# Kernel tuning notes

Measured on AMD Instinct MI355X. Metric: run time of the kernel, lower is better.

## Reference

```python
import jax, jax.numpy as jnp
import numpy as np

B, T, D, H = 4, 2048, 512, 8
DK = D // H

def setup_inputs() -> dict:
    key = jax.random.key(0)
    ks = jax.random.split(key, 5)
    s = 1.0 / np.sqrt(D)
    return {
        "x": jax.random.normal(ks[0], (B, T, D), dtype=jnp.float32),
        "Wq": jax.random.normal(ks[1], (D, D), dtype=jnp.float32) * s,
        "bq": jnp.zeros((D,), dtype=jnp.float32),
        "Wk": jax.random.normal(ks[2], (D, D), dtype=jnp.float32) * s,
        "bk": jnp.zeros((D,), dtype=jnp.float32),
        "Wv": jax.random.normal(ks[3], (D, D), dtype=jnp.float32) * s,
        "bv": jnp.zeros((D,), dtype=jnp.float32),
        "Wo": jax.random.normal(ks[4], (D, D), dtype=jnp.float32) * s,
        "bo": jnp.zeros((D,), dtype=jnp.float32),
    }

def reference(x, Wq, bq, Wk, bk, Wv, bv, Wo, bo):
    # Linear projections (torch Linear: x @ W.T + b); split into heads.
    q = (x @ Wq.T + bq).reshape(B, T, H, DK)  # [B,T,H,dk]
    k = (x @ Wk.T + bk).reshape(B, T, H, DK)
    v = (x @ Wv.T + bv).reshape(B, T, H, DK)
    scale = 1.0 / np.sqrt(DK)
    # scores: [B,H,T,T]
    scores = jnp.einsum("bqhd,bkhd->bhqk", q, k) * scale
    attn = jax.nn.softmax(scores, axis=-1)
    ctx = jnp.einsum("bhqk,bkhd->bqhd", attn, v).reshape(B, T, D)
    return ctx @ Wo.T + bo
```

## Files before the change

### kernel.cpp

```cpp
#include <hip/hip_runtime.h>
#include <stdint.h>

#define NB 4
#define NT 2048
#define ND 512
#define NH 8
#define NDK 64
#define NM (NB*NT)

typedef __attribute__((ext_vector_type(8))) short short8;
typedef __attribute__((ext_vector_type(4))) short bs4;
typedef __attribute__((ext_vector_type(4))) float f32x4;

__device__ __forceinline__ unsigned short f2b(float f) {
    union { float f; uint32_t u; } v; v.f = f;
    return (unsigned short)((v.u + 0x7FFFu + ((v.u >> 16) & 1u)) >> 16);
}

__device__ __forceinline__ void load_lds16(const void* g, void* l) {
    void* gn = const_cast<void*>(g);
    __builtin_amdgcn_global_load_lds((__attribute__((address_space(1))) void*)gn,
                                     (__attribute__((address_space(3))) void*)l,
                                     16, 0, 0);
}

__global__ void convert_all(const float* __restrict__ x,  const float* __restrict__ wq,
                            const float* __restrict__ wk, const float* __restrict__ wv,
                            const float* __restrict__ wo, unsigned short* __restrict__ dst) {
    size_t i = ((size_t)blockIdx.x * 256 + threadIdx.x) * 4;
    const float* src; size_t off;
    if (i < 4194304) { src = x; off = i; }
    else {
        size_t j = i - 4194304;
        src = (j < 262144) ? wq : (j < 524288) ? wk : (j < 786432) ? wv : wo;
        off = j & 262143;
    }
    f32x4 v = *(const f32x4*)(src + off);
    ushort4 r;
    r.x = f2b(v[0]); r.y = f2b(v[1]); r.z = f2b(v[2]); r.w = f2b(v[3]);
    *(ushort4*)(dst + i) = r;
}

__global__ __launch_bounds__(256, 3) void proj_gemm(
        const unsigned short* __restrict__ X,
        const unsigned short* __restrict__ Wbase,
        const float* __restrict__ bias0, const float* __restrict__ bias1,
        const float* __restrict__ bias2,
        unsigned short* __restrict__ Obase, unsigned short* __restrict__ VTb,
        float scale0) {
    const int z = blockIdx.z;
    const float* bias = (z == 0) ? bias0 : (z == 1 ? bias1 : bias2);
    const float scale = (z == 0) ? scale0 : 1.0f;

    int rowBase, colBase;
    const unsigned short *Ap, *Bp;
    if (z == 2) {
        rowBase = blockIdx.x * 128;  colBase = blockIdx.y * 128;
        Ap = Wbase + 2 * (ND * ND);  Bp = X;
    } else {
        rowBase = blockIdx.y * 128;  colBase = blockIdx.x * 128;
        Ap = X;                      Bp = Wbase + (size_t)z * (ND * ND);
    }

    __shared__ alignas(16) unsigned short ldsA[128 * 32];
    __shared__ alignas(16) unsigned short ldsW[128 * 32];

    const int tid = threadIdx.x;
    const int lane = tid & 63, wave = tid >> 6;
    const int quad = lane >> 4, l15 = lane & 15;
    const int wm = wave >> 1, wn = wave & 1;

    const int rS = wave * 16 + (lane >> 2);
    const int kS = (lane & 3) * 8;
    const unsigned short* gA = Ap + (size_t)(rowBase + rS) * ND + kS;
    const unsigned short* gW = Bp + (size_t)(colBase + rS) * ND + kS;
    unsigned short* lA = ldsA + wave * 512;
    unsigned short* lW = ldsW + wave * 512;

    f32x4 acc[4][4];
#pragma unroll
    for (int i = 0; i < 4; i++)
#pragma unroll
        for (int j = 0; j < 4; j++) acc[i][j] = (f32x4)0.0f;

    for (int kt = 0; kt < ND / 32; ++kt) {
        __syncthreads();
        load_lds16(gA,            lA);
        load_lds16(gA + 64 * ND,  lA + 2048);
        load_lds16(gW,            lW);
        load_lds16(gW + 64 * ND,  lW + 2048);
        gA += 32; gW += 32;
        __syncthreads();

        short8 af[4], bfm[4];
#pragma unroll
        for (int mt = 0; mt < 4; ++mt)
            af[mt] = *(const short8*)(ldsA + (wm * 64 + mt * 16 + l15) * 32 + quad * 8);
#pragma unroll
        for (int nt = 0; nt < 4; ++nt)
            bfm[nt] = *(const short8*)(ldsW + (wn * 64 + nt * 16 + l15) * 32 + quad * 8);
#pragma unroll
        for (int mt = 0; mt < 4; ++mt)
#pragma unroll
            for (int nt = 0; nt < 4; ++nt)
                acc[mt][nt] = __builtin_amdgcn_mfma_f32_16x16x32_bf16(
                    af[mt], bfm[nt], acc[mt][nt], 0, 0, 0);
    }

    if (z == 2) {
        const int bz = colBase >> 11;
        const int t0 = colBase & 2047;
        unsigned short* VTo = VTb + ((size_t)(bz * 512 + rowBase)) * NT + t0;
#pragma unroll
        for (int mt = 0; mt < 4; mt++)
#pragma unroll
            for (int reg = 0; reg < 4; reg++) {
                int m = wm * 64 + mt * 16 + quad * 4 + reg;
                float bm = bias[rowBase + m];
                unsigned short* dst = VTo + (size_t)m * NT + wn * 64 + l15;
#pragma unroll
                for (int nt = 0; nt < 4; nt++)
                    dst[nt * 16] = f2b(acc[mt][nt][reg] + bm);
            }
    } else {
        float biasr[4];
#pragma unroll
        for (int nt = 0; nt < 4; nt++)
            biasr[nt] = bias[colBase + wn * 64 + nt * 16 + l15];
        unsigned short* Oz = Obase + (size_t)z * ((size_t)NM * ND);
#pragma unroll
        for (int mt = 0; mt < 4; mt++) {
            int row = rowBase + wm * 64 + mt * 16 + quad * 4;
#pragma unroll
            for (int reg = 0; reg < 4; reg++) {
                unsigned short* dst = Oz + (size_t)(row + reg) * ND + colBase + wn * 64 + l15;
#pragma unroll
                for (int nt = 0; nt < 4; nt++)
                    dst[nt * 16] = f2b((acc[mt][nt][reg] + biasr[nt]) * scale);
            }
        }
    }
}

__global__ __launch_bounds__(256, 4) void out_gemm(
        const unsigned short* __restrict__ A, const unsigned short* __restrict__ W,
        const float* __restrict__ bias, float* __restrict__ OF) {
    __shared__ alignas(16) unsigned short ldsA[64 * 32];
    __shared__ alignas(16) unsigned short ldsW[128 * 32];

    const int tid = threadIdx.x;
    const int lane = tid & 63, wave = tid >> 6;
    const int quad = lane >> 4, l15 = lane & 15;
    const int rowBase = blockIdx.y * 64;
    const int colBase = blockIdx.x * 128;

    const int rW = wave * 16 + (lane >> 2);
    const int kS = (lane & 3) * 8;
    const unsigned short* gA = A + (size_t)(rowBase + rW) * ND + kS;
    const unsigned short* gW = W + (size_t)(colBase + rW) * ND + kS;
    unsigned short* lA = ldsA + wave * 512;
    unsigned short* lW = ldsW + wave * 512;

    f32x4 acc[8];
#pragma unroll
    for (int nt = 0; nt < 8; nt++) acc[nt] = (f32x4)0.0f;

    for (int kt = 0; kt < ND / 32; ++kt) {
        __syncthreads();
        load_lds16(gA,           lA);
        load_lds16(gW,           lW);
        load_lds16(gW + 64 * ND, lW + 2048);
        gA += 32; gW += 32;
        __syncthreads();

        short8 af = *(const short8*)(ldsA + (wave * 16 + l15) * 32 + quad * 8);
#pragma unroll
        for (int nt = 0; nt < 8; ++nt) {
            short8 bfm = *(const short8*)(ldsW + (nt * 16 + l15) * 32 + quad * 8);
            acc[nt] = __builtin_amdgcn_mfma_f32_16x16x32_bf16(af, bfm, acc[nt], 0, 0, 0);
        }
    }

    float biasr[8];
#pragma unroll
    for (int nt = 0; nt < 8; nt++)
        biasr[nt] = bias[colBase + nt * 16 + l15];

#pragma unroll
    for (int reg = 0; reg < 4; reg++) {
        int row = rowBase + wave * 16 + quad * 4 + reg;
        float* dst = OF + (size_t)row * ND + colBase + l15;
#pragma unroll
        for (int nt = 0; nt < 8; nt++)
            dst[nt * 16] = acc[nt][reg] + biasr[nt];
    }
}

__global__ __launch_bounds__(256, 4) void attn_kernel(
        const unsigned short* __restrict__ Qb, const unsigned short* __restrict__ Kb,
        const unsigned short* __restrict__ VTb, unsigned short* __restrict__ Cb) {
    const int qt = blockIdx.x, h = blockIdx.y, b = blockIdx.z;
    __shared__ alignas(16) unsigned short Ks[64 * 64];
    __shared__ alignas(16) unsigned short Vt[64 * 64];

    const int tid = threadIdx.x, lane = tid & 63, wave = tid >> 6;
    const int quad = lane >> 4, l15 = lane & 15;
    const size_t headOff = (size_t)h * NDK;
    const size_t rowB = (size_t)b * NT;
    const unsigned short* VT = VTb + (size_t)(b * NH + h) * ((size_t)NDK * NT);

    short8 aq[2];
#pragma unroll
    for (int ks = 0; ks < 2; ++ks)
        aq[ks] = *(const short8*)(Qb + (rowB + qt * 64 + wave * 16 + l15) * ND
                                  + headOff + ks * 32 + quad * 8);

    const int r0 = wave * 16 + (lane >> 3);
    const int g0 = (lane & 7) ^ (r0 & 7);
    const unsigned short* Kbh = Kb + rowB * ND + headOff;
    const size_t offK0 = (size_t)r0 * ND + g0 * 8;
    const size_t offK1 = (size_t)(r0 + 8) * ND + g0 * 8;
    const size_t offV0 = (size_t)r0 * NT + g0 * 8;
    const size_t offV1 = (size_t)(r0 + 8) * NT + g0 * 8;
    unsigned short* ldsK = Ks + wave * 1024;
    unsigned short* ldsV = Vt + wave * 1024;

    const int swz = (l15 & 7);

    f32x4 o[4];
#pragma unroll
    for (int nt = 0; nt < 4; nt++) o[nt] = (f32x4)0.0f;
    float lacc = 0.0f;

    for (int kv = 0; kv < NT / 64; ++kv) {
        const unsigned short* kb = Kbh + (size_t)kv * 64 * ND;
        const unsigned short* vb = VT + kv * 64;
        __syncthreads();
        load_lds16(kb + offK0, ldsK);
        load_lds16(kb + offK1, ldsK + 512);
        load_lds16(vb + offV0, ldsV);
        load_lds16(vb + offV1, ldsV + 512);
        __syncthreads();

        bs4 pk[4];
#pragma unroll
        for (int kt = 0; kt < 4; ++kt) {
            f32x4 st = (f32x4)0.0f;
#pragma unroll
            for (int ks = 0; ks < 2; ++ks) {
                short8 ak = *(const short8*)&Ks[(kt * 16 + l15) * 64
                                                + (((ks * 4 + quad) ^ swz) * 8)];
                st = __builtin_amdgcn_mfma_f32_16x16x32_bf16(ak, aq[ks], st, 0, 0, 0);
            }
            float p0 = exp2f(st[0]), p1 = exp2f(st[1]);
            float p2 = exp2f(st[2]), p3 = exp2f(st[3]);
            lacc += (p0 + p1) + (p2 + p3);
            uint32_t lo = __builtin_amdgcn_perm(__float_as_uint(p1), __float_as_uint(p0),
                                                0x07060302u);
            uint32_t hi = __builtin_amdgcn_perm(__float_as_uint(p3), __float_as_uint(p2),
                                                0x07060302u);
            union { uint32_t w[2]; bs4 v; } cvt;
            cvt.w[0] = lo; cvt.w[1] = hi;
            pk[kt] = cvt.v;
        }

#pragma unroll
        for (int kt = 0; kt < 4; ++kt)
#pragma unroll
            for (int nt = 0; nt < 4; ++nt) {
                int cc = kt * 2 + (quad >> 1);
                bs4 vbf = *(const bs4*)&Vt[(nt * 16 + l15) * 64
                                           + ((cc ^ swz) * 8) + (quad & 1) * 4];
                o[nt] = __builtin_amdgcn_mfma_f32_16x16x16bf16_1k(pk[kt], vbf, o[nt], 0, 0, 0);
            }
    }

    lacc += __shfl_xor(lacc, 16);
    lacc += __shfl_xor(lacc, 32);

#pragma unroll
    for (int reg = 0; reg < 4; ++reg) {
        float inv = 1.0f / __shfl(lacc, quad * 4 + reg);
        size_t row = rowB + qt * 64 + wave * 16 + quad * 4 + reg;
#pragma unroll
        for (int nt = 0; nt < 4; ++nt)
            Cb[row * ND + headOff + nt * 16 + l15] = f2b(o[nt][reg] * inv);
    }
}

extern "C" void kernel_launch(void* const* d_in, const int* in_sizes, int n_in,
                              void* d_out, int out_size, void* d_ws, size_t ws_size,
                              hipStream_t stream) {
    (void)in_sizes; (void)n_in; (void)out_size; (void)ws_size;
    const float* x  = (const float*)d_in[0];
    const float* Wq = (const float*)d_in[1];
    const float* bq = (const float*)d_in[2];
    const float* Wk = (const float*)d_in[3];
    const float* bk = (const float*)d_in[4];
    const float* Wv = (const float*)d_in[5];
    const float* bv = (const float*)d_in[6];
    const float* Wo = (const float*)d_in[7];
    const float* bo = (const float*)d_in[8];
    float* out = (float*)d_out;

    unsigned short* ws  = (unsigned short*)d_ws;
    unsigned short* xb  = ws;
    unsigned short* wqb = xb + 4194304;
    unsigned short* Qb  = wqb + 4 * 262144;
    unsigned short* Kb  = Qb + 4194304;
    unsigned short* VTb = Kb + 4194304;
    unsigned short* Cb  = VTb + 4194304;
    unsigned short* wob = wqb + 3 * 262144;

    convert_all<<<5120, 256, 0, stream>>>(x, Wq, Wk, Wv, Wo, ws);

    const float qscale = 0.125f * 1.44269504f;
    proj_gemm<<<dim3(4, 64, 3), 256, 0, stream>>>(xb, wqb, bq, bk, bv, Qb, VTb, qscale);
    attn_kernel<<<dim3(32, 8, 4), 256, 0, stream>>>(Qb, Kb, VTb, Cb);
    out_gemm<<<dim3(4, 128), 256, 0, stream>>>(Cb, wob, bo, out);
}
```

Measured before the change: 178.5 us.

## Double-buffer K/V tiles in attention and use 2x2 wave tiling in output GEMM

The attention kernel now keeps two LDS buffers for K and V^T and prefetches the next 64-key tile while the current one is consumed. Only one barrier per iteration remains, so global-to-LDS latency can overlap with the MFMA and exp work. Separately, the output-projection GEMM changes its per-wave tiling from 16x128 to 32x64. This cuts redundant LDS fragment reads per MFMA. The cost is doubled attention LDS use (32KB per block) and the risk that the compiler inserts conservative vmcnt waits that serialize the prefetch.

```diff
diff --git a/kernel.cpp b/kernel.cpp
--- a/kernel.cpp
+++ b/kernel.cpp
@@ -151,6 +151,7 @@
     const int tid = threadIdx.x;
     const int lane = tid & 63, wave = tid >> 6;
     const int quad = lane >> 4, l15 = lane & 15;
+    const int wm = wave >> 1, wn = wave & 1;
     const int rowBase = blockIdx.y * 64;
     const int colBase = blockIdx.x * 128;
 
@@ -161,9 +162,11 @@
     unsigned short* lA = ldsA + wave * 512;
     unsigned short* lW = ldsW + wave * 512;
 
-    f32x4 acc[8];
-#pragma unroll
-    for (int nt = 0; nt < 8; nt++) acc[nt] = (f32x4)0.0f;
+    f32x4 acc[2][4];
+#pragma unroll
+    for (int mt = 0; mt < 2; mt++)
+#pragma unroll
+        for (int nt = 0; nt < 4; nt++) acc[mt][nt] = (f32x4)0.0f;
 
     for (int kt = 0; kt < ND / 32; ++kt) {
         __syncthreads();
@@ -173,35 +176,44 @@
         gA += 32; gW += 32;
         __syncthreads();
 
-        short8 af = *(const short8*)(ldsA + (wave * 16 + l15) * 32 + quad * 8);
-#pragma unroll
-        for (int nt = 0; nt < 8; ++nt) {
-            short8 bfm = *(const short8*)(ldsW + (nt * 16 + l15) * 32 + quad * 8);
-            acc[nt] = __builtin_amdgcn_mfma_f32_16x16x32_bf16(af, bfm, acc[nt], 0, 0, 0);
+        short8 af[2], bfm[4];
+#pragma unroll
+        for (int mt = 0; mt < 2; ++mt)
+            af[mt] = *(const short8*)(ldsA + (wm * 32 + mt * 16 + l15) * 32 + quad * 8);
+#pragma unroll
+        for (int nt = 0; nt < 4; ++nt)
+            bfm[nt] = *(const short8*)(ldsW + (wn * 64 + nt * 16 + l15) * 32 + quad * 8);
+#pragma unroll
+        for (int mt = 0; mt < 2; ++mt)
+#pragma unroll
+            for (int nt = 0; nt < 4; ++nt)
+                acc[mt][nt] = __builtin_amdgcn_mfma_f32_16x16x32_bf16(
+                    af[mt], bfm[nt], acc[mt][nt], 0, 0, 0);
+    }
+
+    float biasr[4];
+#pragma unroll
+    for (int nt = 0; nt < 4; nt++)
+        biasr[nt] = bias[colBase + wn * 64 + nt * 16 + l15];
+
+#pragma unroll
+    for (int mt = 0; mt < 2; mt++)
+#pragma unroll
+        for (int reg = 0; reg < 4; reg++) {
+            int row = rowBase + wm * 32 + mt * 16 + quad * 4 + reg;
+            float* dst = OF + (size_t)row * ND + colBase + wn * 64 + l15;
+#pragma unroll
+            for (int nt = 0; nt < 4; nt++)
+                dst[nt * 16] = acc[mt][nt][reg] + biasr[nt];
         }
-    }
-
-    float biasr[8];
-#pragma unroll
-    for (int nt = 0; nt < 8; nt++)
-        biasr[nt] = bias[colBase + nt * 16 + l15];
-
-#pragma unroll
-    for (int reg = 0; reg < 4; reg++) {
-        int row = rowBase + wave * 16 + quad * 4 + reg;
-        float* dst = OF + (size_t)row * ND + colBase + l15;
-#pragma unroll
-        for (int nt = 0; nt < 8; nt++)
-            dst[nt * 16] = acc[nt][reg] + biasr[nt];
-    }
 }
 
 __global__ __launch_bounds__(256, 4) void attn_kernel(
         const unsigned short* __restrict__ Qb, const unsigned short* __restrict__ Kb,
         const unsigned short* __restrict__ VTb, unsigned short* __restrict__ Cb) {
     const int qt = blockIdx.x, h = blockIdx.y, b = blockIdx.z;
-    __shared__ alignas(16) unsigned short Ks[64 * 64];
-    __shared__ alignas(16) unsigned short Vt[64 * 64];
+    __shared__ alignas(16) unsigned short Ks[2 * 64 * 64];
+    __shared__ alignas(16) unsigned short Vt[2 * 64 * 64];
 
     const int tid = threadIdx.x, lane = tid & 63, wave = tid >> 6;
     const int quad = lane >> 4, l15 = lane & 15;
@@ -222,8 +234,6 @@
     const size_t offK1 = (size_t)(r0 + 8) * ND + g0 * 8;
     const size_t offV0 = (size_t)r0 * NT + g0 * 8;
     const size_t offV1 = (size_t)(r0 + 8) * NT + g0 * 8;
-    unsigned short* ldsK = Ks + wave * 1024;
-    unsigned short* ldsV = Vt + wave * 1024;
 
     const int swz = (l15 & 7);
 
@@ -232,15 +242,31 @@
     for (int nt = 0; nt < 4; nt++) o[nt] = (f32x4)0.0f;
     float lacc = 0.0f;
 
+    {
+        unsigned short* dK = Ks + wave * 1024;
+        unsigned short* dV = Vt + wave * 1024;
+        load_lds16(Kbh + offK0, dK);
+        load_lds16(Kbh + offK1, dK + 512);
+        load_lds16(VT + offV0, dV);
+        load_lds16(VT + offV1, dV + 512);
+    }
+
     for (int kv = 0; kv < NT / 64; ++kv) {
-        const unsigned short* kb = Kbh + (size_t)kv * 64 * ND;
-        const unsigned short* vb = VT + kv * 64;
-        __syncthreads();
-        load_lds16(kb + offK0, ldsK);
-        load_lds16(kb + offK1, ldsK + 512);
-        load_lds16(vb + offV0, ldsV);
-        load_lds16(vb + offV1, ldsV + 512);
-        __syncthreads();
+        __syncthreads();
+
+        if (kv + 1 < NT / 64) {
+            const unsigned short* kb = Kbh + (size_t)(kv + 1) * 64 * ND;
+            const unsigned short* vb = VT + (kv + 1) * 64;
+            unsigned short* dK = Ks + ((kv + 1) & 1) * 4096 + wave * 1024;
+            unsigned short* dV = Vt + ((kv + 1) & 1) * 4096 + wave * 1024;
+            load_lds16(kb + offK0, dK);
+            load_lds16(kb + offK1, dK + 512);
+            load_lds16(vb + offV0, dV);
+            load_lds16(vb + offV1, dV + 512);
+        }
+
+        const unsigned short* KsC = Ks + (kv & 1) * 4096;
+        const unsigned short* VtC = Vt + (kv & 1) * 4096;
 
         bs4 pk[4];
 #pragma unroll
@@ -248,8 +274,8 @@
             f32x4 st = (f32x4)0.0f;
 #pragma unroll
             for (int ks = 0; ks < 2; ++ks) {
-                short8 ak = *(const short8*)&Ks[(kt * 16 + l15) * 64
-                                                + (((ks * 4 + quad) ^ swz) * 8)];
+                short8 ak = *(const short8*)&KsC[(kt * 16 + l15) * 64
+                                                 + (((ks * 4 + quad) ^ swz) * 8)];
                 st = __builtin_amdgcn_mfma_f32_16x16x32_bf16(ak, aq[ks], st, 0, 0, 0);
             }
             float p0 = exp2f(st[0]), p1 = exp2f(st[1]);
@@ -269,8 +295,8 @@
 #pragma unroll
             for (int nt = 0; nt < 4; ++nt) {
                 int cc = kt * 2 + (quad >> 1);
-                bs4 vbf = *(const bs4*)&Vt[(nt * 16 + l15) * 64
-                                           + ((cc ^ swz) * 8) + (quad & 1) * 4];
+                bs4 vbf = *(const bs4*)&VtC[(nt * 16 + l15) * 64
+                                            + ((cc ^ swz) * 8) + (quad & 1) * 4];
                 o[nt] = __builtin_amdgcn_mfma_f32_16x16x16bf16_1k(pk[kt], vbf, o[nt], 0, 0, 0);
             }
     }
```

After: 180.4 us. No clear change (+1.1%).
